# Kernel optimization log

Hardware: AMD Instinct MI355X
Metric: run time of the kernel (lower is better)

Reference implementation:

```python
import jax, jax.numpy as jnp
import numpy as np

# ---- constants (from init_kwargs / Box defaults) ----
B, K, T = 32768, 256, 10
C_LIGHT, F0, DF = 3.0e8, 1.0e10, 3.0e4
D_EL = C_LIGHT / (2.0 * F0)            # half-wavelength spacing
SPATIAL = F0 * D_EL / C_LIGHT          # = 0.5
RANGE_C = 2.0 * DF / C_LIGHT           # = 2e-4
THETA_MIN, THETA_MAX = -60.0, 60.0
R_MIN, R_MAX = 0.0, 2000.0
BETA = 2.0
STEP_CLIP = 0.1
INIT_ALPHA, INIT_LAMBDA = 0.01, 0.001
ALPHA_MIN, ALPHA_MAX = 1e-6, 0.2
LAM_MIN, LAM_MAX = 1e-6, 1.0
EPS = 1e-6


def _atanh(y):
    return jnp.arctanh(jnp.clip(y, -1.0 + EPS, 1.0 - EPS))


def map_theta_r_to_u(theta_deg, r_m):
    mid = 0.5 * (THETA_MIN + THETA_MAX)
    half = 0.5 * (THETA_MAX - THETA_MIN)
    y = (theta_deg - mid) / half
    s = jnp.clip((r_m - R_MIN) / (R_MAX - R_MIN), EPS, 1.0 - EPS)
    u_r = _atanh(2.0 * s - 1.0)          # tanh r_box inverse
    return jnp.stack([_atanh(y), u_r], axis=-1)  # (B,2)


def map_u_to_theta_r(u):
    mid = 0.5 * (THETA_MIN + THETA_MAX)
    half = 0.5 * (THETA_MAX - THETA_MIN)
    theta = mid + half * jnp.tanh(u[:, 0])
    s = 0.5 * (jnp.tanh(u[:, 1]) + 1.0)
    r = R_MIN + (R_MAX - R_MIN) * s
    return theta, r


def steering(theta_deg, r_m):
    # FDA steering: phase_k = 2*pi*k*(0.5*sin(theta) - 2*df*r/c)
    k = jnp.arange(K, dtype=jnp.float32)
    th = theta_deg * (jnp.pi / 180.0)
    phase = (2.0 * jnp.pi) * k[None, :] * (
        SPATIAL * jnp.sin(th)[:, None] - RANGE_C * r_m[:, None])  # (B,K)
    inv_sqrt_k = 1.0 / np.sqrt(K)
    return jnp.cos(phase) * inv_sqrt_k, jnp.sin(phase) * inv_sqrt_k


def loglike_logistic(theta_deg, r_m, z_re, z_im):
    # 1-bit logistic log-likelihood, summed over array elements -> (B,)
    a_re, a_im = steering(theta_deg, r_m)
    ll = jax.nn.log_sigmoid(BETA * z_re * a_re) + jax.nn.log_sigmoid(BETA * z_im * a_im)
    return jnp.sum(ll, axis=-1)


def setup_inputs() -> dict:
    key = jax.random.key(0)
    k1, k2, k3, k4 = jax.random.split(key, 4)
    z_real = jnp.sign(jax.random.normal(k1, (B, K), dtype=jnp.float32))
    z_imag = jnp.sign(jax.random.normal(k2, (B, K), dtype=jnp.float32))
    theta0 = jax.random.uniform(k3, (B,), jnp.float32, -55.0, 55.0)
    r0 = jax.random.uniform(k4, (B,), jnp.float32, 100.0, 1900.0)
    a_raw0 = float(np.log(np.expm1(INIT_ALPHA)))   # inverse softplus
    l_raw0 = float(np.log(np.expm1(INIT_LAMBDA)))
    return {
        "z_real": z_real, "z_imag": z_imag,
        "theta0_deg": theta0, "r0_m": r0,
        "alpha_theta_raw": jnp.full((T,), a_raw0, jnp.float32),
        "alpha_r_raw": jnp.full((T,), a_raw0, jnp.float32),
        "lambda_theta_raw": jnp.full((T,), l_raw0, jnp.float32),
        "lambda_r_raw": jnp.full((T,), l_raw0, jnp.float32),
    }


def reference(z_real, z_imag, theta0_deg, r0_m,
              alpha_theta_raw, alpha_r_raw, lambda_theta_raw, lambda_r_raw):
    alpha_th = jnp.clip(jax.nn.softplus(alpha_theta_raw), ALPHA_MIN, ALPHA_MAX)
    alpha_r = jnp.clip(jax.nn.softplus(alpha_r_raw), ALPHA_MIN, ALPHA_MAX)
    lam_th = jnp.clip(jax.nn.softplus(lambda_theta_raw), LAM_MIN, LAM_MAX)
    lam_r = jnp.clip(jax.nn.softplus(lambda_r_raw), LAM_MIN, LAM_MAX)

    u0 = map_theta_r_to_u(theta0_deg, r0_m)  # (B,2)

    def neg_obj_sum(u):
        th, r = map_u_to_theta_r(u)
        return -jnp.sum(loglike_logistic(th, r, z_real, z_imag))

    grad_fn = jax.grad(neg_obj_sum)

    def body(u, params):
        a_th, a_r, l_th, l_r = params
        # first-order unroll: gradient is a constant w.r.t. outer autodiff
        g = jax.lax.stop_gradient(grad_fn(u))
        g = jnp.where(jnp.isfinite(g), g, 0.0)
        g_th, g_r = g[:, 0], g[:, 1]
        a_th = jnp.where(jnp.isfinite(a_th), a_th, INIT_ALPHA)
        a_r = jnp.where(jnp.isfinite(a_r), a_r, INIT_ALPHA)
        l_th = jnp.where(jnp.isfinite(l_th), l_th, INIT_LAMBDA)
        l_r = jnp.where(jnp.isfinite(l_r), l_r, INIT_LAMBDA)
        den_th = jnp.maximum(jnp.nan_to_num(
            jnp.maximum(jnp.abs(g_th), 1e-6) + l_th, nan=1.0, posinf=1.0, neginf=1.0), 1e-6)
        den_r = jnp.maximum(jnp.nan_to_num(
            jnp.maximum(jnp.abs(g_r), 1e-6) + l_r, nan=1.0, posinf=1.0, neginf=1.0), 1e-6)
        step_u = jnp.stack([a_th * g_th / den_th, a_r * g_r / den_r], axis=-1)
        step_u = jnp.clip(jnp.nan_to_num(step_u, nan=0.0, posinf=0.0, neginf=0.0),
                          -STEP_CLIP, STEP_CLIP)
        return u - step_u, None

    uT, _ = jax.lax.scan(body, u0, (alpha_th, alpha_r, lam_th, lam_r))
    theta_T, r_T = map_u_to_theta_r(uT)
    return jnp.stack([theta_T, r_T], axis=-1)  # (B,2)
```

## Files before the change

### kernel.cpp

```cpp
#include <hip/hip_runtime.h>
#include <cstdint>

#define PI_F 3.14159265358979323846f

__device__ __forceinline__ float fract_(float x)  { return __builtin_amdgcn_fractf(x); }
__device__ __forceinline__ float sin2pi_(float r) { return __builtin_amdgcn_sinf(r); }
__device__ __forceinline__ float cos2pi_(float r) { return __builtin_amdgcn_cosf(r); }

extern "C" __global__ void __launch_bounds__(256)
pack_signs(const float4* __restrict__ zr, const float4* __restrict__ zi,
           uint32_t* __restrict__ pr, uint32_t* __restrict__ pim) {
    const int t = blockIdx.x * 256 + threadIdx.x;
    uint32_t wr = 0u, wi = 0u;
    #pragma unroll
    for (int q = 0; q < 8; ++q) {
        const float4 a = zr[t * 8 + q];
        const float4 b = zi[t * 8 + q];
        wr |= ((uint32_t)(a.x < 0.f) << (4 * q))     | ((uint32_t)(a.y < 0.f) << (4 * q + 1))
            | ((uint32_t)(a.z < 0.f) << (4 * q + 2)) | ((uint32_t)(a.w < 0.f) << (4 * q + 3));
        wi |= ((uint32_t)(b.x < 0.f) << (4 * q))     | ((uint32_t)(b.y < 0.f) << (4 * q + 1))
            | ((uint32_t)(b.z < 0.f) << (4 * q + 2)) | ((uint32_t)(b.w < 0.f) << (4 * q + 3));
    }
    pr[t] = wr;
    pim[t] = wi;
}

extern "C" __global__ void __launch_bounds__(512, 4)
refine(const float* __restrict__ th0, const float* __restrict__ r0,
       const float* __restrict__ a_th_raw, const float* __restrict__ a_r_raw,
       const float* __restrict__ l_th_raw, const float* __restrict__ l_r_raw,
       const uint32_t* __restrict__ pr, const uint32_t* __restrict__ pim,
       float* __restrict__ out) {
    const int tid  = threadIdx.x;
    const int lane = tid & 63;
    const int wv   = tid >> 6;
    const int w_   = wv >> 1;
    const int mA   = 2 * (wv & 1);
    const int item = blockIdx.x * 64 + lane;

    __shared__ float sp[4][10];
    __shared__ float red[2][8][64];

    if (tid < 40) {
        const int a = tid / 10, i = tid % 10;
        const float* src = (a == 0) ? a_th_raw : (a == 1) ? a_r_raw
                         : (a == 2) ? l_th_raw : l_r_raw;
        const float v  = log1pf(expf(src[i]));
        const float hi = (a < 2) ? 0.2f : 1.0f;
        sp[a][i] = fminf(fmaxf(v, 1e-6f), hi);
    }

    const uint32_t br0 = pr [item * 8 + w_ * 2 + 0];
    const uint32_t br1 = pr [item * 8 + w_ * 2 + 1];
    const uint32_t bi0 = pim[item * 8 + w_ * 2 + 0];
    const uint32_t bi1 = pim[item * 8 + w_ * 2 + 1];

    float y = th0[item] * (1.0f / 60.0f);
    y = fminf(fmaxf(y, -1.0f + 1e-6f), 1.0f - 1e-6f);
    float u0 = atanhf(y);
    float sR = r0[item] * (1.0f / 2000.0f);
    sR = fminf(fmaxf(sR, 1e-6f), 1.0f - 1e-6f);
    float u1 = atanhf(2.0f * sR - 1.0f);

    const float w64 = (float)(w_ * 64);

    __syncthreads();

    for (int t = 0; t < 10; ++t) {
        const float ath = sp[0][t], ar = sp[1][t], lth = sp[2][t], lr = sp[3][t];

        const float T0 = tanhf(u0), T1 = tanhf(u1);
        const float th_rad = (PI_F / 3.0f) * T0;
        const float sth = sinf(th_rad), cth = cosf(th_rad);
        const float r   = 1000.0f * (T1 + 1.0f);
        const float crev = 0.5f * sth - 2e-4f * r;

        const float d4 = fract_(4.0f * crev);
        const float C4 = cos2pi_(d4), S4 = sin2pi_(d4);

        float c[2], s[2], kf[2], acc[2];
        #pragma unroll
        for (int mm = 0; mm < 2; ++mm) {
            const float k0 = w64 + (float)(mA + mm);
            const float rv = fract_(k0 * crev);
            c[mm]   = cos2pi_(rv);
            s[mm]   = sin2pi_(rv);
            kf[mm]  = k0;
            acc[mm] = 0.0f;
        }

        #pragma unroll
        for (int j = 0; j < 16; ++j) {
            #pragma unroll
            for (int mm = 0; mm < 2; ++mm) {
                const int kl = (mA + mm) + 4 * j;
                const uint32_t wr = (kl < 32) ? br0 : br1;
                const uint32_t wi = (kl < 32) ? bi0 : bi1;
                const int sh = 31 - (kl & 31);
                const uint32_t mre = (wr << sh) & 0x80000000u;
                const uint32_t mim = (wi << sh) & 0x80000000u;
                const float cs = c[mm], ss = s[mm];
                const float zc = __uint_as_float(__float_as_uint(cs) ^ mim);
                const float zs = __uint_as_float(__float_as_uint(ss) ^ mre);
                const float w0 = zc - zs;
                const float u2 = ss * ss;
                const float t2 = fmaf(-2.0f, u2, 1.0f);
                const float sc = ss * cs;
                const float v  = sc * t2;
                const float Wk = fmaf(v, -(1.0f / 196608.0f), w0 * 0.0625f);
                acc[mm] = fmaf(kf[mm], Wk, acc[mm]);
                kf[mm] += 4.0f;
                const float tA = ss * S4;
                const float tB = cs * S4;
                c[mm] = fmaf(cs, C4, -tA);
                s[mm] = fmaf(ss, C4, tB);
            }
        }

        const int p = t & 1;
        red[p][wv][lane] = acc[0] + acc[1];
        __syncthreads();

        const float S0 = red[p][0][lane] + red[p][1][lane];
        const float S1 = red[p][2][lane] + red[p][3][lane];
        const float S2 = red[p][4][lane] + red[p][5][lane];
        const float S3 = red[p][6][lane] + red[p][7][lane];
        const float S  = (S0 + S1) + (S2 + S3);

        const float g0 = -(PI_F * PI_F / 3.0f) * cth * (1.0f - T0 * T0) * S;
        const float g1 = 0.4f * PI_F * (1.0f - T1 * T1) * S;
        const float den0 = fmaxf(fabsf(g0), 1e-6f) + lth;
        const float den1 = fmaxf(fabsf(g1), 1e-6f) + lr;
        float st0 = ath * g0 / den0;
        float st1 = ar  * g1 / den1;
        st0 = fminf(fmaxf(st0, -0.1f), 0.1f);
        st1 = fminf(fmaxf(st1, -0.1f), 0.1f);
        u0 -= st0;
        u1 -= st1;
    }

    if (wv == 0) {
        const float thT = 60.0f * tanhf(u0);
        const float rT  = 1000.0f * (tanhf(u1) + 1.0f);
        reinterpret_cast<float2*>(out)[item] = make_float2(thT, rT);
    }
}

extern "C" void kernel_launch(void* const* d_in, const int* in_sizes, int n_in,
                              void* d_out, int out_size, void* d_ws, size_t ws_size,
                              hipStream_t stream) {
    const float* zr   = (const float*)d_in[0];
    const float* zi   = (const float*)d_in[1];
    const float* th0  = (const float*)d_in[2];
    const float* r0   = (const float*)d_in[3];
    const float* athr = (const float*)d_in[4];
    const float* arr  = (const float*)d_in[5];
    const float* lthr = (const float*)d_in[6];
    const float* lrr  = (const float*)d_in[7];

    const int B  = in_sizes[2];
    const int BK = in_sizes[0];

    uint32_t* pr  = (uint32_t*)d_ws;
    uint32_t* pim = pr + (size_t)B * 8;

    pack_signs<<<(BK / 32) / 256, 256, 0, stream>>>((const float4*)zr, (const float4*)zi,
                                                    pr, pim);
    refine<<<B / 64, 512, 0, stream>>>(th0, r0, athr, arr, lthr, lrr, pr, pim,
                                       (float*)d_out);
}
```

Measured before the change: 147.9 us.

## Fuse sign packing into refine kernel and add dedicated scalar-update wave

Merges the sign-packing pass into the refine kernel: each block packs the signs for its 64 items into shared memory instead of writing them to a workspace and reading them back in a second launch. A ninth wavefront is added that owns the per-item scalar state (u, tanh, sin/cos) and publishes the next iteration's phase parameters through a double-buffered shared array, so the eight compute waves no longer redundantly evaluate the transcendentals. The cost is a second barrier per iteration, an idle ninth wave during the inner loop, a larger block (576 threads) with lower occupancy bounds, and a serial dependency on the update wave between iterations.

```diff
diff --git a/kernel.cpp b/kernel.cpp
--- a/kernel.cpp
+++ b/kernel.cpp
@@ -7,142 +7,173 @@
 __device__ __forceinline__ float sin2pi_(float r) { return __builtin_amdgcn_sinf(r); }
 __device__ __forceinline__ float cos2pi_(float r) { return __builtin_amdgcn_cosf(r); }
 
-extern "C" __global__ void __launch_bounds__(256)
-pack_signs(const float4* __restrict__ zr, const float4* __restrict__ zi,
-           uint32_t* __restrict__ pr, uint32_t* __restrict__ pim) {
-    const int t = blockIdx.x * 256 + threadIdx.x;
-    uint32_t wr = 0u, wi = 0u;
-    #pragma unroll
-    for (int q = 0; q < 8; ++q) {
-        const float4 a = zr[t * 8 + q];
-        const float4 b = zi[t * 8 + q];
-        wr |= ((uint32_t)(a.x < 0.f) << (4 * q))     | ((uint32_t)(a.y < 0.f) << (4 * q + 1))
-            | ((uint32_t)(a.z < 0.f) << (4 * q + 2)) | ((uint32_t)(a.w < 0.f) << (4 * q + 3));
-        wi |= ((uint32_t)(b.x < 0.f) << (4 * q))     | ((uint32_t)(b.y < 0.f) << (4 * q + 1))
-            | ((uint32_t)(b.z < 0.f) << (4 * q + 2)) | ((uint32_t)(b.w < 0.f) << (4 * q + 3));
+extern "C" __global__ void __launch_bounds__(576, 2)
+refine_fused(const float4* __restrict__ zr4, const float4* __restrict__ zi4,
+             const float* __restrict__ th0, const float* __restrict__ r0,
+             const float* __restrict__ a_th_raw, const float* __restrict__ a_r_raw,
+             const float* __restrict__ l_th_raw, const float* __restrict__ l_r_raw,
+             float* __restrict__ out) {
+    const int tid   = threadIdx.x;
+    const int lane  = tid & 63;
+    const int wv    = tid >> 6;
+    const int item0 = blockIdx.x * 64;
+
+    __shared__ uint32_t s_pr[64][8];
+    __shared__ uint32_t s_pi[64][8];
+    __shared__ float    sp[4][10];
+    __shared__ float    bc[2][3][64];
+    __shared__ float    red[2][8][64];
+
+    float u0 = 0.0f, u1 = 0.0f, T0 = 0.0f, T1 = 0.0f, cth = 0.0f;
+
+    if (wv < 8) {
+        const int it = tid >> 3, wd = tid & 7;
+        const size_t f4 = (size_t)(item0 + it) * 64 + (size_t)wd * 8;
+        uint32_t wr = 0u, wi = 0u;
+        #pragma unroll
+        for (int q = 0; q < 8; ++q) {
+            const float4 a = zr4[f4 + q];
+            const float4 b = zi4[f4 + q];
+            wr |= ((uint32_t)(a.x < 0.f) << (4 * q))     | ((uint32_t)(a.y < 0.f) << (4 * q + 1))
+                | ((uint32_t)(a.z < 0.f) << (4 * q + 2)) | ((uint32_t)(a.w < 0.f) << (4 * q + 3));
+            wi |= ((uint32_t)(b.x < 0.f) << (4 * q))     | ((uint32_t)(b.y < 0.f) << (4 * q + 1))
+                | ((uint32_t)(b.z < 0.f) << (4 * q + 2)) | ((uint32_t)(b.w < 0.f) << (4 * q + 3));
+        }
+        s_pr[it][wd] = wr;
+        s_pi[it][wd] = wi;
+    } else {
+        if (lane < 40) {
+            const int a = lane / 10, i = lane % 10;
+            const float* src = (a == 0) ? a_th_raw : (a == 1) ? a_r_raw
+                             : (a == 2) ? l_th_raw : l_r_raw;
+            const float v  = log1pf(expf(src[i]));
+            const float hi = (a < 2) ? 0.2f : 1.0f;
+            sp[a][i] = fminf(fmaxf(v, 1e-6f), hi);
+        }
+        const int item = item0 + lane;
+        float y = th0[item] * (1.0f / 60.0f);
+        y = fminf(fmaxf(y, -1.0f + 1e-6f), 1.0f - 1e-6f);
+        u0 = atanhf(y);
+        float sR = r0[item] * (1.0f / 2000.0f);
+        sR = fminf(fmaxf(sR, 1e-6f), 1.0f - 1e-6f);
+        u1 = atanhf(2.0f * sR - 1.0f);
+
+        T0 = tanhf(u0);
+        T1 = tanhf(u1);
+        const float th_rad = (PI_F / 3.0f) * T0;
+        const float sth = sinf(th_rad);
+        cth = cosf(th_rad);
+        const float r    = 1000.0f * (T1 + 1.0f);
+        const float crev = 0.5f * sth - 2e-4f * r;
+        const float d4   = fract_(4.0f * crev);
+        bc[0][0][lane] = crev;
+        bc[0][1][lane] = cos2pi_(d4);
+        bc[0][2][lane] = sin2pi_(d4);
     }
-    pr[t] = wr;
-    pim[t] = wi;
-}
+    __syncthreads();
 
-extern "C" __global__ void __launch_bounds__(512, 4)
-refine(const float* __restrict__ th0, const float* __restrict__ r0,
-       const float* __restrict__ a_th_raw, const float* __restrict__ a_r_raw,
-       const float* __restrict__ l_th_raw, const float* __restrict__ l_r_raw,
-       const uint32_t* __restrict__ pr, const uint32_t* __restrict__ pim,
-       float* __restrict__ out) {
-    const int tid  = threadIdx.x;
-    const int lane = tid & 63;
-    const int wv   = tid >> 6;
-    const int w_   = wv >> 1;
-    const int mA   = 2 * (wv & 1);
-    const int item = blockIdx.x * 64 + lane;
+    const int w_ = wv >> 1;
+    const int mA = 2 * (wv & 1);
+    uint32_t br0 = 0, br1 = 0, bi0 = 0, bi1 = 0;
+    if (wv < 8) {
+        br0 = s_pr[lane][2 * w_ + 0];
+        br1 = s_pr[lane][2 * w_ + 1];
+        bi0 = s_pi[lane][2 * w_ + 0];
+        bi1 = s_pi[lane][2 * w_ + 1];
+    }
+    const float w64 = (float)(w_ * 64);
 
-    __shared__ float sp[4][10];
-    __shared__ float red[2][8][64];
+    for (int t = 0; t < 10; ++t) {
+        const int p = t & 1;
 
-    if (tid < 40) {
-        const int a = tid / 10, i = tid % 10;
-        const float* src = (a == 0) ? a_th_raw : (a == 1) ? a_r_raw
-                         : (a == 2) ? l_th_raw : l_r_raw;
-        const float v  = log1pf(expf(src[i]));
-        const float hi = (a < 2) ? 0.2f : 1.0f;
-        sp[a][i] = fminf(fmaxf(v, 1e-6f), hi);
+        if (wv < 8) {
+            const float crev = bc[p][0][lane];
+            const float C4   = bc[p][1][lane];
+            const float S4   = bc[p][2][lane];
+
+            float c[2], s[2], kf[2], acc[2];
+            #pragma unroll
+            for (int mm = 0; mm < 2; ++mm) {
+                const float k0 = w64 + (float)(mA + mm);
+                const float rv = fract_(k0 * crev);
+                c[mm]   = cos2pi_(rv);
+                s[mm]   = sin2pi_(rv);
+                kf[mm]  = k0;
+                acc[mm] = 0.0f;
+            }
+
+            #pragma unroll
+            for (int j = 0; j < 16; ++j) {
+                #pragma unroll
+                for (int mm = 0; mm < 2; ++mm) {
+                    const int kl = (mA + mm) + 4 * j;
+                    const uint32_t wr = (kl < 32) ? br0 : br1;
+                    const uint32_t wi = (kl < 32) ? bi0 : bi1;
+                    const int sh = 31 - (kl & 31);
+                    const uint32_t mre = (wr << sh) & 0x80000000u;
+                    const uint32_t mim = (wi << sh) & 0x80000000u;
+                    const float cs = c[mm], ss = s[mm];
+                    const float zc = __uint_as_float(__float_as_uint(cs) ^ mim);
+                    const float zs = __uint_as_float(__float_as_uint(ss) ^ mre);
+                    const float w0 = zc - zs;
+                    const float u2 = ss * ss;
+                    const float t2 = fmaf(-2.0f, u2, 1.0f);
+                    const float sc = ss * cs;
+                    const float v  = sc * t2;
+                    const float Wk = fmaf(v, -(1.0f / 196608.0f), w0 * 0.0625f);
+                    acc[mm] = fmaf(kf[mm], Wk, acc[mm]);
+                    kf[mm] += 4.0f;
+                    const float tA = ss * S4;
+                    const float tB = cs * S4;
+                    c[mm] = fmaf(cs, C4, -tA);
+                    s[mm] = fmaf(ss, C4, tB);
+                }
+            }
+            red[p][wv][lane] = acc[0] + acc[1];
+        }
+        __syncthreads();
+
+        if (wv == 8) {
+            const float S0 = red[p][0][lane] + red[p][1][lane];
+            const float S1 = red[p][2][lane] + red[p][3][lane];
+            const float S2 = red[p][4][lane] + red[p][5][lane];
+            const float S3 = red[p][6][lane] + red[p][7][lane];
+            const float S  = (S0 + S1) + (S2 + S3);
+
+            const float ath = sp[0][t], ar = sp[1][t], lth = sp[2][t], lr = sp[3][t];
+
+            const float g0 = -(PI_F * PI_F / 3.0f) * cth * (1.0f - T0 * T0) * S;
+            const float g1 = 0.4f * PI_F * (1.0f - T1 * T1) * S;
+            const float den0 = fmaxf(fabsf(g0), 1e-6f) + lth;
+            const float den1 = fmaxf(fabsf(g1), 1e-6f) + lr;
+            float st0 = ath * g0 / den0;
+            float st1 = ar  * g1 / den1;
+            st0 = fminf(fmaxf(st0, -0.1f), 0.1f);
+            st1 = fminf(fmaxf(st1, -0.1f), 0.1f);
+            u0 -= st0;
+            u1 -= st1;
+
+            if (t < 9) {
+                T0 = tanhf(u0);
+                T1 = tanhf(u1);
+                const float th_rad = (PI_F / 3.0f) * T0;
+                const float sth = sinf(th_rad);
+                cth = cosf(th_rad);
+                const float r     = 1000.0f * (T1 + 1.0f);
+                const float crevN = 0.5f * sth - 2e-4f * r;
+                const float d4    = fract_(4.0f * crevN);
+                bc[p ^ 1][0][lane] = crevN;
+                bc[p ^ 1][1][lane] = cos2pi_(d4);
+                bc[p ^ 1][2][lane] = sin2pi_(d4);
+            }
+        }
+        __syncthreads();
     }
 
-    const uint32_t br0 = pr [item * 8 + w_ * 2 + 0];
-    const uint32_t br1 = pr [item * 8 + w_ * 2 + 1];
-    const uint32_t bi0 = pim[item * 8 + w_ * 2 + 0];
-    const uint32_t bi1 = pim[item * 8 + w_ * 2 + 1];
-
-    float y = th0[item] * (1.0f / 60.0f);
-    y = fminf(fmaxf(y, -1.0f + 1e-6f), 1.0f - 1e-6f);
-    float u0 = atanhf(y);
-    float sR = r0[item] * (1.0f / 2000.0f);
-    sR = fminf(fmaxf(sR, 1e-6f), 1.0f - 1e-6f);
-    float u1 = atanhf(2.0f * sR - 1.0f);
-
-    const float w64 = (float)(w_ * 64);
-
-    __syncthreads();
-
-    for (int t = 0; t < 10; ++t) {
-        const float ath = sp[0][t], ar = sp[1][t], lth = sp[2][t], lr = sp[3][t];
-
-        const float T0 = tanhf(u0), T1 = tanhf(u1);
-        const float th_rad = (PI_F / 3.0f) * T0;
-        const float sth = sinf(th_rad), cth = cosf(th_rad);
-        const float r   = 1000.0f * (T1 + 1.0f);
-        const float crev = 0.5f * sth - 2e-4f * r;
-
-        const float d4 = fract_(4.0f * crev);
-        const float C4 = cos2pi_(d4), S4 = sin2pi_(d4);
-
-        float c[2], s[2], kf[2], acc[2];
-        #pragma unroll
-        for (int mm = 0; mm < 2; ++mm) {
-            const float k0 = w64 + (float)(mA + mm);
-            const float rv = fract_(k0 * crev);
-            c[mm]   = cos2pi_(rv);
-            s[mm]   = sin2pi_(rv);
-            kf[mm]  = k0;
-            acc[mm] = 0.0f;
-        }
-
-        #pragma unroll
-        for (int j = 0; j < 16; ++j) {
-            #pragma unroll
-            for (int mm = 0; mm < 2; ++mm) {
-                const int kl = (mA + mm) + 4 * j;
-                const uint32_t wr = (kl < 32) ? br0 : br1;
-                const uint32_t wi = (kl < 32) ? bi0 : bi1;
-                const int sh = 31 - (kl & 31);
-                const uint32_t mre = (wr << sh) & 0x80000000u;
-                const uint32_t mim = (wi << sh) & 0x80000000u;
-                const float cs = c[mm], ss = s[mm];
-                const float zc = __uint_as_float(__float_as_uint(cs) ^ mim);
-                const float zs = __uint_as_float(__float_as_uint(ss) ^ mre);
-                const float w0 = zc - zs;
-                const float u2 = ss * ss;
-                const float t2 = fmaf(-2.0f, u2, 1.0f);
-                const float sc = ss * cs;
-                const float v  = sc * t2;
-                const float Wk = fmaf(v, -(1.0f / 196608.0f), w0 * 0.0625f);
-                acc[mm] = fmaf(kf[mm], Wk, acc[mm]);
-                kf[mm] += 4.0f;
-                const float tA = ss * S4;
-                const float tB = cs * S4;
-                c[mm] = fmaf(cs, C4, -tA);
-                s[mm] = fmaf(ss, C4, tB);
-            }
-        }
-
-        const int p = t & 1;
-        red[p][wv][lane] = acc[0] + acc[1];
-        __syncthreads();
-
-        const float S0 = red[p][0][lane] + red[p][1][lane];
-        const float S1 = red[p][2][lane] + red[p][3][lane];
-        const float S2 = red[p][4][lane] + red[p][5][lane];
-        const float S3 = red[p][6][lane] + red[p][7][lane];
-        const float S  = (S0 + S1) + (S2 + S3);
-
-        const float g0 = -(PI_F * PI_F / 3.0f) * cth * (1.0f - T0 * T0) * S;
-        const float g1 = 0.4f * PI_F * (1.0f - T1 * T1) * S;
-        const float den0 = fmaxf(fabsf(g0), 1e-6f) + lth;
-        const float den1 = fmaxf(fabsf(g1), 1e-6f) + lr;
-        float st0 = ath * g0 / den0;
-        float st1 = ar  * g1 / den1;
-        st0 = fminf(fmaxf(st0, -0.1f), 0.1f);
-        st1 = fminf(fmaxf(st1, -0.1f), 0.1f);
-        u0 -= st0;
-        u1 -= st1;
-    }
-
-    if (wv == 0) {
+    if (wv == 8) {
         const float thT = 60.0f * tanhf(u0);
         const float rT  = 1000.0f * (tanhf(u1) + 1.0f);
-        reinterpret_cast<float2*>(out)[item] = make_float2(thT, rT);
+        reinterpret_cast<float2*>(out)[item0 + lane] = make_float2(thT, rT);
     }
 }
 
@@ -158,14 +189,9 @@
     const float* lthr = (const float*)d_in[6];
     const float* lrr  = (const float*)d_in[7];
 
-    const int B  = in_sizes[2];
-    const int BK = in_sizes[0];
+    const int B = in_sizes[2];
 
-    uint32_t* pr  = (uint32_t*)d_ws;
-    uint32_t* pim = pr + (size_t)B * 8;
-
-    pack_signs<<<(BK / 32) / 256, 256, 0, stream>>>((const float4*)zr, (const float4*)zi,
-                                                    pr, pim);
-    refine<<<B / 64, 512, 0, stream>>>(th0, r0, athr, arr, lthr, lrr, pr, pim,
-                                       (float*)d_out);
+    refine_fused<<<B / 64, 576, 0, stream>>>((const float4*)zr, (const float4*)zi,
+                                             th0, r0, athr, arr, lthr, lrr,
+                                             (float*)d_out);
 }
```

Measured after the change: 148.2 us. Within noise of the previous version (+0.2%).
